# Performance work log

Hardware: AMD Instinct MI355X
Metric: run time of the kernel (lower is better)

The kernel has to match this reference:

```python
import jax, jax.numpy as jnp
import numpy as np
import math

NUM_HEADS = 8
Q_STRIDE = 2
KV_STRIDE = 2
POS_MAG = 1.0
WAVE_LEN = 1000.0


def _pos_embedding(h, w, h_kv, w_kv, feat_dim):
    # sinusoidal embedding of coordinate differences (in input-resolution units)
    h_idxs = jnp.arange(h, dtype=jnp.float32) * Q_STRIDE
    w_idxs = jnp.arange(w, dtype=jnp.float32) * Q_STRIDE
    h_kv_idxs = jnp.arange(h_kv, dtype=jnp.float32) * KV_STRIDE
    w_kv_idxs = jnp.arange(w_kv, dtype=jnp.float32) * KV_STRIDE
    h_diff = (h_idxs[:, None] - h_kv_idxs[None, :]) * POS_MAG  # [h, h_kv]
    w_diff = (w_idxs[:, None] - w_kv_idxs[None, :]) * POS_MAG  # [w, w_kv]
    feat_range = jnp.arange(feat_dim // 4, dtype=jnp.float32)
    dim_mat = WAVE_LEN ** (4.0 / feat_dim * feat_range)       # [feat_dim/4]
    ang_x = w_diff[:, :, None] / dim_mat                       # [w, w_kv, feat_dim/4]
    ang_y = h_diff[:, :, None] / dim_mat                       # [h, h_kv, feat_dim/4]
    emb_x = jnp.concatenate([jnp.sin(ang_x), jnp.cos(ang_x)], axis=2)  # [w, w_kv, feat_dim/2]
    emb_y = jnp.concatenate([jnp.sin(ang_y), jnp.cos(ang_y)], axis=2)  # [h, h_kv, feat_dim/2]
    return emb_x, emb_y


def setup_inputs() -> dict:
    key = jax.random.key(0)
    ks = jax.random.split(key, 10)
    n, C, H, W = 2, 256, 96, 96
    s = 0.05
    return {
        "x": jax.random.normal(ks[0], (n, C, H, W), jnp.float32),
        "Wq": jax.random.normal(ks[1], (C, C), jnp.float32) * s,
        "Wk": jax.random.normal(ks[2], (C, C), jnp.float32) * s,
        "Wv": jax.random.normal(ks[3], (C, C), jnp.float32) * s,
        "Wx": jax.random.normal(ks[4], (C, C // 2), jnp.float32) * s,
        "Wy": jax.random.normal(ks[5], (C, C // 2), jnp.float32) * s,
        "appr_bias": jax.random.normal(ks[6], (C,), jnp.float32) * s,
        "Wp": jax.random.normal(ks[7], (C, C), jnp.float32) * s,
        "bp": jax.random.normal(ks[8], (C,), jnp.float32) * s,
        "gamma": jax.random.normal(ks[9], (1,), jnp.float32),
    }


def reference(x, Wq, Wk, Wv, Wx, Wy, appr_bias, Wp, bp, gamma):
    n, C, H, W = x.shape
    g = NUM_HEADS
    d = C // g  # qk_embed_dim == v_dim
    # AvgPool2d(kernel_size=1, stride=s) == strided subsampling
    x_q = x[:, :, ::Q_STRIDE, ::Q_STRIDE]
    x_kv = x[:, :, ::KV_STRIDE, ::KV_STRIDE]
    h, w = x_q.shape[2], x_q.shape[3]
    h_kv, w_kv = x_kv.shape[2], x_kv.shape[3]

    # 1x1 convs (no bias) == channel matmuls
    q = jnp.einsum('oc,nchw->nohw', Wq, x_q)   # [n, C, h, w]
    k = jnp.einsum('oc,nchw->nohw', Wk, x_kv)  # [n, C, h_kv, w_kv]
    v = jnp.einsum('oc,nchw->nohw', Wv, x_kv)  # [n, C, h_kv, w_kv]

    emb_x, emb_y = _pos_embedding(h, w, h_kv, w_kv, C)
    inv_sqrt2 = 1.0 / math.sqrt(2.0)
    # Linear(feat_dim/2 -> C), split into heads, scale by 1/sqrt(2)
    pos_x = (jnp.einsum('wvf,of->wvo', emb_x, Wx).reshape(w, w_kv, g, d)
             .transpose(2, 0, 1, 3)) * inv_sqrt2  # [g, w, w_kv, d]
    pos_y = (jnp.einsum('huf,of->huo', emb_y, Wy).reshape(h, h_kv, g, d)
             .transpose(2, 0, 1, 3)) * inv_sqrt2  # [g, h, h_kv, d]

    qr = q.reshape(n, g, d, h, w).transpose(0, 1, 3, 4, 2)  # [n, g, h, w, d]
    kr = k.reshape(n, g, d, h_kv * w_kv)                     # [n, g, d, kv]

    # bias . key term, broadcast over query positions
    e_key = jnp.einsum('gd,ngdk->ngk', appr_bias.reshape(g, d), kr)
    e_key = e_key.reshape(n, g, 1, 1, h_kv, w_kv)
    # query . pos_x term (broadcast over h_kv), query . pos_y term (broadcast over w_kv)
    e_x = jnp.einsum('nghwd,gwvd->nghwv', qr, pos_x)[:, :, :, :, None, :]
    e_y = jnp.einsum('nghwd,ghud->nghwu', qr, pos_y)[:, :, :, :, :, None]

    energy = (e_key + e_x + e_y).reshape(n, g, h * w, h_kv * w_kv)
    attn = jax.nn.softmax(energy, axis=-1)  # [n, g, hw, kv]

    vr = v.reshape(n, g, d, h_kv * w_kv)  # [n, g, d, kv]
    out = jnp.einsum('ngqk,ngdk->ngdq', attn, vr).reshape(n, C, h, w)

    out = jnp.einsum('oc,nchw->nohw', Wp, out) + bp[None, :, None, None]
    out = jax.image.resize(out, (n, C, H, W), method='bilinear')
    return gamma * out + x
```

## Files before the change

### kernel.cpp

```cpp
#include <hip/hip_runtime.h>
#include <hip/hip_bf16.h>
#include <math.h>

#define NB 2
#define CC 256
#define NPOS 2304
#define NDELTA 95

typedef __attribute__((ext_vector_type(8))) short short8;
typedef __attribute__((ext_vector_type(4))) float floatx4;

__device__ inline unsigned short f2bf(float x) {
    unsigned int u = __float_as_uint(x);
    u = (u + 0x7FFFu + ((u >> 16) & 1u)) >> 16;
    return (unsigned short)u;
}
__device__ inline float bf2f(unsigned short h) {
    return __uint_as_float(((unsigned int)h) << 16);
}
__device__ inline unsigned int pk2(float a, float b) {
    return (unsigned int)f2bf(a) | ((unsigned int)f2bf(b) << 16);
}
__device__ inline unsigned int pkmul(unsigned int a, unsigned int b) {
    __hip_bfloat162 x = *(__hip_bfloat162*)&a;
    __hip_bfloat162 y = *(__hip_bfloat162*)&b;
    __hip_bfloat162 r = __hmul2(x, y);
    return *(unsigned int*)&r;
}

__global__ __launch_bounds__(256) void prep_extract_kernel(
    const float* __restrict__ Wx, const float* __restrict__ Wy,
    const float* __restrict__ Wk, const float* __restrict__ ab,
    const float* __restrict__ Wq, const float* __restrict__ Wv,
    const float* __restrict__ Wp, const float* __restrict__ x,
    unsigned short* __restrict__ posxb, unsigned short* __restrict__ posyb,
    unsigned short* __restrict__ Wb, unsigned short* __restrict__ Wpb,
    unsigned short* __restrict__ xs_t)
{
    __shared__ __align__(16) unsigned short Lt[64][264];
    int b = blockIdx.x;
    int t = threadIdx.x;
    if (b < NDELTA) {
        float* emb = (float*)&Lt[0][0];
        float delta = (float)(b - 47);
        if (t < 64) {
            float dim_inv = exp2f(-(float)t * 0.15571537944784511f);
            float ang = 2.0f * delta * dim_inv;
            emb[t]      = sinf(ang);
            emb[t + 64] = cosf(ang);
        }
        __syncthreads();
        float4 sx4 = {0.f,0.f,0.f,0.f}, sy4 = {0.f,0.f,0.f,0.f};
        const float4* wxr = (const float4*)(Wx + t * 128);
        const float4* wyr = (const float4*)(Wy + t * 128);
        const float4* e4  = (const float4*)emb;
        for (int f = 0; f < 32; ++f) {
            float4 e = e4[f], a = wxr[f], bb = wyr[f];
            sx4.x += e.x * a.x;  sx4.y += e.y * a.y;
            sx4.z += e.z * a.z;  sx4.w += e.w * a.w;
            sy4.x += e.x * bb.x; sy4.y += e.y * bb.y;
            sy4.z += e.z * bb.z; sy4.w += e.w * bb.w;
        }
        float sx = (sx4.x + sx4.y) + (sx4.z + sx4.w);
        float sy = (sy4.x + sy4.y) + (sy4.z + sy4.w);
        const float inv_sqrt2 = 0.70710678118654752440f;
        int g = t >> 5, d = t & 31;
        posxb[((size_t)g * 96 + b) * 32 + d] = f2bf(sx * inv_sqrt2);
        posyb[((size_t)g * 96 + b) * 32 + d] = f2bf(sy * inv_sqrt2);
    } else if (b == NDELTA) {
        int g = t >> 5, d = t & 31;
        posxb[((size_t)g * 96 + 95) * 32 + d] = 0;
        posyb[((size_t)g * 96 + 95) * 32 + d] = 0;
    } else if (b < 96 + 640) {
        int o = b - 96;
        float v = 0.f;
        if (o < 256)      v = Wq[o * 256 + t];
        else if (o < 512) v = Wv[(o - 256) * 256 + t];
        else if (o < 520) {
            int g = o - 512;
            float s = 0.f;
            for (int d = 0; d < 32; ++d)
                s += ab[g * 32 + d] * Wk[(g * 32 + d) * 256 + t];
            v = s;
        }
        Wb[(size_t)o * 256 + t] = f2bf(v);
    } else if (b < 992) {
        int o = b - 736;
        Wpb[(size_t)o * 256 + t] = f2bf(Wp[o * 256 + t]);
    } else {
        int blk = b - 992;
        int pt = blk % 36;
        int n = blk / 36;
        int p0 = pt * 64;
        int cw = t >> 4;
        int pl = t & 15;

        for (int cc = 0; cc < 16; ++cc) {
            int c = cc * 16 + cw;
            const float* src = x + ((size_t)(n * 256 + c)) * (96 * 96);
            #pragma unroll
            for (int k = 0; k < 4; ++k) {
                int p = p0 + pl + k * 16;
                int i = p / 48, j = p - i * 48;
                Lt[pl + k * 16][c] = f2bf(src[(2 * i) * 96 + 2 * j]);
            }
        }
        __syncthreads();
        #pragma unroll
        for (int it = 0; it < 8; ++it) {
            int s = t + it * 256;
            int p = s >> 5, c8 = s & 31;
            uint4 v = *(const uint4*)&Lt[p][c8 * 8];
            *(uint4*)(xs_t + ((size_t)(n * NPOS + p0 + p)) * 256 + c8 * 8) = v;
        }
    }
}

__global__ __launch_bounds__(256, 2) void qkvh_kernel(
    const unsigned short* __restrict__ xs_t, const unsigned short* __restrict__ Wb,
    unsigned short* __restrict__ qbuf, uint4* __restrict__ vhat)
{
    __shared__ __align__(16) unsigned short Vt[4][33][72];
    int mT = blockIdx.x;
    int nT = blockIdx.y;
    int t = threadIdx.x;
    int wm = t >> 6, L = t & 63, l16 = L & 15, oct = L >> 4;
    int colBase = nT * 64;
    int n = colBase / NPOS;
    int p0 = colBase - n * NPOS;
    int o_w = mT * 128 + wm * 32;
    bool isV = (mT >= 2);
    int gv = (mT & 1) * 4 + wm;

    const unsigned short* A0 = Wb + (size_t)(o_w + l16) * 256 + oct * 8;
    const unsigned short* A1 = A0 + 16 * 256;
    const unsigned short* AE = Wb + (size_t)(512 + gv) * 256 + oct * 8;
    const unsigned short* B0 = xs_t + ((size_t)(n * NPOS + p0 + l16)) * 256 + oct * 8;

    floatx4 acc[2][4] = {};
    floatx4 accE[4] = {};
    #pragma unroll
    for (int kc = 0; kc < 8; ++kc) {
        int k0 = kc * 32;
        short8 a0 = *(const short8*)(A0 + k0);
        short8 a1 = *(const short8*)(A1 + k0);
        short8 b0 = *(const short8*)(B0 + k0);
        short8 b1 = *(const short8*)(B0 + 16 * 256 + k0);
        short8 b2 = *(const short8*)(B0 + 32 * 256 + k0);
        short8 b3 = *(const short8*)(B0 + 48 * 256 + k0);
        acc[0][0] = __builtin_amdgcn_mfma_f32_16x16x32_bf16(a0, b0, acc[0][0], 0, 0, 0);
        acc[0][1] = __builtin_amdgcn_mfma_f32_16x16x32_bf16(a0, b1, acc[0][1], 0, 0, 0);
        acc[0][2] = __builtin_amdgcn_mfma_f32_16x16x32_bf16(a0, b2, acc[0][2], 0, 0, 0);
        acc[0][3] = __builtin_amdgcn_mfma_f32_16x16x32_bf16(a0, b3, acc[0][3], 0, 0, 0);
        acc[1][0] = __builtin_amdgcn_mfma_f32_16x16x32_bf16(a1, b0, acc[1][0], 0, 0, 0);
        acc[1][1] = __builtin_amdgcn_mfma_f32_16x16x32_bf16(a1, b1, acc[1][1], 0, 0, 0);
        acc[1][2] = __builtin_amdgcn_mfma_f32_16x16x32_bf16(a1, b2, acc[1][2], 0, 0, 0);
        acc[1][3] = __builtin_amdgcn_mfma_f32_16x16x32_bf16(a1, b3, acc[1][3], 0, 0, 0);
        if (isV) {
            short8 ae = *(const short8*)(AE + k0);
            accE[0] = __builtin_amdgcn_mfma_f32_16x16x32_bf16(ae, b0, accE[0], 0, 0, 0);
            accE[1] = __builtin_amdgcn_mfma_f32_16x16x32_bf16(ae, b1, accE[1], 0, 0, 0);
            accE[2] = __builtin_amdgcn_mfma_f32_16x16x32_bf16(ae, b2, accE[2], 0, 0, 0);
            accE[3] = __builtin_amdgcn_mfma_f32_16x16x32_bf16(ae, b3, accE[3], 0, 0, 0);
        }
    }

    if (!isV) {
        #pragma unroll
        for (int af = 0; af < 2; ++af) {
            int ob = o_w + af * 16 + oct * 4;
            int gq = ob >> 5, d0 = ob & 31;
            #pragma unroll
            for (int f = 0; f < 4; ++f) {
                int p = p0 + f * 16 + l16;
                uint2 w;
                w.x = pk2(acc[af][f][0], acc[af][f][1]);
                w.y = pk2(acc[af][f][2], acc[af][f][3]);
                *(uint2*)&qbuf[((size_t)(n * 8 + gq) * NPOS + p) * 32 + d0] = w;
            }
        }
    } else {
        #pragma unroll
        for (int f = 0; f < 4; ++f) {
            float e = __expf(accE[f][0]);
            #pragma unroll
            for (int af = 0; af < 2; ++af)
                #pragma unroll
                for (int r = 0; r < 4; ++r)
                    Vt[wm][af * 16 + oct * 4 + r][f * 16 + l16] =
                        f2bf(acc[af][f][r] * e);
            if (oct == 0)
                Vt[wm][32][f * 16 + l16] = f2bf(e);
        }
        __syncthreads();

        int i = L >> 3, j = L & 7;
        int K = p0 + 8 * i;
        int tile = K / 96;
        int rem = K - tile * 96;
        int cc = rem >> 5;
        int lhi = (rem & 31) >> 3;
        uint4* vout = vhat + ((size_t)(n * 8 + gv) * 24 + tile) * 576;
        #pragma unroll
        for (int mm = 0; mm < 4; ++mm) {
            int d = j + 8 * mm;
            int nn = d >> 4;
            int Ls = lhi * 16 + (d & 15);
            uint4 w = *(const uint4*)&Vt[wm][d][8 * i];
            vout[(cc * 3 + nn) * 64 + Ls] = w;
        }
        {
            uint4 wa = (j == 0) ? *(const uint4*)&Vt[wm][32][8 * i]
                                : make_uint4(0u, 0u, 0u, 0u);
            vout[(cc * 3 + 2) * 64 + lhi * 16 + j] = wa;
            vout[(cc * 3 + 2) * 64 + lhi * 16 + j + 8] = make_uint4(0u, 0u, 0u, 0u);
        }
    }
}

#define DO_TILE(BB, TT) do {                                                   \
    int u0_ = (TT) * 2;                                                        \
    unsigned int y0_ = Ys[qp * 50 + u0_];     y0_ |= y0_ << 16;                \
    unsigned int y1_ = Ys[qp * 50 + u0_ + 1]; y1_ |= y1_ << 16;                \
    unsigned int Yc0_ = y0_, Yc1_ = (o < 2) ? y0_ : y1_, Yc2_ = y1_;           \
    union { unsigned int u[4]; short8 s; } av_;                                \
    av_.u[0] = pkmul(Xp[0], Yc0_); av_.u[1] = pkmul(Xp[1], Yc0_);              \
    av_.u[2] = pkmul(Xp[2], Yc0_); av_.u[3] = pkmul(Xp[3], Yc0_);              \
    acc0 = __builtin_amdgcn_mfma_f32_16x16x32_bf16(av_.s, *(const short8*)&BB[0], acc0, 0, 0, 0); \
    acc1 = __builtin_amdgcn_mfma_f32_16x16x32_bf16(av_.s, *(const short8*)&BB[1], acc1, 0, 0, 0); \
    acc2 = __builtin_amdgcn_mfma_f32_16x16x32_bf16(av_.s, *(const short8*)&BB[2], acc2, 0, 0, 0); \
    av_.u[0] = pkmul(Xp[4], Yc1_); av_.u[1] = pkmul(Xp[5], Yc1_);              \
    av_.u[2] = pkmul(Xp[6], Yc1_); av_.u[3] = pkmul(Xp[7], Yc1_);              \
    acc0 = __builtin_amdgcn_mfma_f32_16x16x32_bf16(av_.s, *(const short8*)&BB[3], acc0, 0, 0, 0); \
    acc1 = __builtin_amdgcn_mfma_f32_16x16x32_bf16(av_.s, *(const short8*)&BB[4], acc1, 0, 0, 0); \
    acc2 = __builtin_amdgcn_mfma_f32_16x16x32_bf16(av_.s, *(const short8*)&BB[5], acc2, 0, 0, 0); \
    av_.u[0] = pkmul(Xp[8], Yc2_); av_.u[1] = pkmul(Xp[9], Yc2_);              \
    av_.u[2] = pkmul(Xp[10], Yc2_); av_.u[3] = pkmul(Xp[11], Yc2_);            \
    acc0 = __builtin_amdgcn_mfma_f32_16x16x32_bf16(av_.s, *(const short8*)&BB[6], acc0, 0, 0, 0); \
    acc1 = __builtin_amdgcn_mfma_f32_16x16x32_bf16(av_.s, *(const short8*)&BB[7], acc1, 0, 0, 0); \
    acc2 = __builtin_amdgcn_mfma_f32_16x16x32_bf16(av_.s, *(const short8*)&BB[8], acc2, 0, 0, 0); \
} while (0)

__global__ __launch_bounds__(256, 3) void attn_kernel(
    const unsigned short* __restrict__ qbuf, const unsigned short* __restrict__ posxb,
    const unsigned short* __restrict__ posyb, const uint4* __restrict__ vhat,
    unsigned short* __restrict__ oattn_t)
{
    __shared__ unsigned short Xs[64 * 50];
    __shared__ unsigned short Ys[64 * 50];
    __shared__ float linv_s[64];

    int blk = blockIdx.x;
    int qt = blk % 36;
    int ng = blk / 36;
    int nb = ng >> 3, g = ng & 7;
    int qbase = qt * 64;
    int t = threadIdx.x;
    int m = t >> 6, L = t & 63;
    int l16 = L & 15, oct = L >> 4;

    {
        int qtile0 = qbase + m * 16;
        int hq = qtile0 / 48;
        int wq0 = qtile0 - hq * 48;
        short8 aq = *(const short8*)(qbuf +
            ((size_t)ng * NPOS + qtile0 + l16) * 32 + oct * 8);
        const unsigned short* pxg = posxb + (size_t)g * 96 * 32;
        const unsigned short* pyg = posyb + (size_t)g * 96 * 32;
        floatx4 zero = {0.f, 0.f, 0.f, 0.f};
        #pragma unroll
        for (int j = 0; j < 6; ++j) {
            int dl = j * 16 + l16;
            short8 bx = *(const short8*)(pxg + (size_t)dl * 32 + oct * 8);
            short8 by = *(const short8*)(pyg + (size_t)dl * 32 + oct * 8);
            floatx4 tx = __builtin_amdgcn_mfma_f32_16x16x32_bf16(aq, bx, zero, 0, 0, 0);
            floatx4 ty = __builtin_amdgcn_mfma_f32_16x16x32_bf16(aq, by, zero, 0, 0, 0);
            int u = hq + 47 - dl;
            bool uok = (u >= 0) && (u < 48);
            #pragma unroll
            for (int r = 0; r < 4; ++r) {
                int ql = oct * 4 + r;
                int v = wq0 + ql + 47 - dl;
                if (v >= 0 && v < 48)
                    Xs[(m * 16 + ql) * 50 + v] = f2bf(__expf(tx[r]));
                if (uok)
                    Ys[(m * 16 + ql) * 50 + u] = f2bf(__expf(ty[r]));
            }
        }
    }
    __syncthreads();

    int qp = m * 16 + l16;
    int o = oct;
    unsigned int Xp[12];
    #pragma unroll
    for (int c = 0; c < 3; ++c)
        #pragma unroll
        for (int jj = 0; jj < 4; ++jj) {
            int k = c * 32 + o * 8 + jj * 2;
            int v0 = (k < 48) ? k : k - 48;
            Xp[c * 4 + jj] = *(const unsigned int*)&Xs[qp * 50 + v0];
        }

    floatx4 acc0 = {0.f, 0.f, 0.f, 0.f};
    floatx4 acc1 = {0.f, 0.f, 0.f, 0.f};
    floatx4 acc2 = {0.f, 0.f, 0.f, 0.f};

    const uint4* vb = vhat + (size_t)ng * 24 * 576 + L;
    uint4 Abuf[9], Bbuf[9];
    #pragma unroll
    for (int gg = 0; gg < 9; ++gg) Abuf[gg] = vb[gg * 64];

    for (int tile = 0; tile < 24; tile += 2) {
        const uint4* sB = vb + (tile + 1) * 576;
        #pragma unroll
        for (int gg = 0; gg < 9; ++gg) Bbuf[gg] = sB[gg * 64];
        DO_TILE(Abuf, tile);
        if (tile + 2 < 24) {
            const uint4* sA = vb + (tile + 2) * 576;
            #pragma unroll
            for (int gg = 0; gg < 9; ++gg) Abuf[gg] = sA[gg * 64];
        }
        DO_TILE(Bbuf, tile + 1);
    }

    if ((L & 15) == 0) {
        int qc = m * 16 + (L >> 4) * 4;
        #pragma unroll
        for (int r = 0; r < 4; ++r)
            linv_s[qc + r] = 1.0f / acc2[r];
    }
    __syncthreads();
    {
        int qc = m * 16 + (L >> 4) * 4;
        int d0 = L & 15;
        #pragma unroll
        for (int r = 0; r < 4; ++r) {
            float lir = linv_s[qc + r];
            size_t row = ((size_t)nb * NPOS + qbase + qc + r) * 256;
            oattn_t[row + g * 32 + d0]      = f2bf(acc0[r] * lir);
            oattn_t[row + g * 32 + 16 + d0] = f2bf(acc1[r] * lir);
        }
    }
}

__global__ __launch_bounds__(256, 2) void proj_kernel(
    const unsigned short* __restrict__ oattn_t, const unsigned short* __restrict__ Wpb,
    const float* __restrict__ bpv, unsigned short* __restrict__ projb)
{
    int mT = blockIdx.x;
    int nT = blockIdx.y;
    int t = threadIdx.x;
    int wm = t >> 6, L = t & 63, l16 = L & 15, oct = L >> 4;
    int colBase = nT * 64;
    int n = colBase / NPOS;
    int p0 = colBase - n * NPOS;
    int o_w = mT * 128 + wm * 32;

    const unsigned short* A0 = Wpb + (size_t)(o_w + l16) * 256 + oct * 8;
    const unsigned short* A1 = A0 + 16 * 256;
    const unsigned short* B0 = oattn_t + ((size_t)(n * NPOS + p0 + l16)) * 256 + oct * 8;

    floatx4 acc[2][4] = {};
    #pragma unroll
    for (int kc = 0; kc < 8; ++kc) {
        int k0 = kc * 32;
        short8 a0 = *(const short8*)(A0 + k0);
        short8 a1 = *(const short8*)(A1 + k0);
        short8 b0 = *(const short8*)(B0 + k0);
        short8 b1 = *(const short8*)(B0 + 16 * 256 + k0);
        short8 b2 = *(const short8*)(B0 + 32 * 256 + k0);
        short8 b3 = *(const short8*)(B0 + 48 * 256 + k0);
        acc[0][0] = __builtin_amdgcn_mfma_f32_16x16x32_bf16(a0, b0, acc[0][0], 0, 0, 0);
        acc[0][1] = __builtin_amdgcn_mfma_f32_16x16x32_bf16(a0, b1, acc[0][1], 0, 0, 0);
        acc[0][2] = __builtin_amdgcn_mfma_f32_16x16x32_bf16(a0, b2, acc[0][2], 0, 0, 0);
        acc[0][3] = __builtin_amdgcn_mfma_f32_16x16x32_bf16(a0, b3, acc[0][3], 0, 0, 0);
        acc[1][0] = __builtin_amdgcn_mfma_f32_16x16x32_bf16(a1, b0, acc[1][0], 0, 0, 0);
        acc[1][1] = __builtin_amdgcn_mfma_f32_16x16x32_bf16(a1, b1, acc[1][1], 0, 0, 0);
        acc[1][2] = __builtin_amdgcn_mfma_f32_16x16x32_bf16(a1, b2, acc[1][2], 0, 0, 0);
        acc[1][3] = __builtin_amdgcn_mfma_f32_16x16x32_bf16(a1, b3, acc[1][3], 0, 0, 0);
    }

    #pragma unroll
    for (int af = 0; af < 2; ++af) {
        #pragma unroll
        for (int f = 0; f < 4; ++f) {
            int p = p0 + f * 16 + l16;
            #pragma unroll
            for (int r = 0; r < 4; ++r) {
                int o = o_w + af * 16 + oct * 4 + r;
                projb[((size_t)(n * 256 + o)) * NPOS + p] = f2bf(acc[af][f][r] + bpv[o]);
            }
        }
    }
}

__global__ __launch_bounds__(256) void resize_kernel(
    const unsigned short* __restrict__ projb, const float* __restrict__ x,
    const float* __restrict__ gamma, float* __restrict__ out)
{
    int idx4 = blockIdx.x * 256 + threadIdx.x;
    int J0 = (idx4 % 24) * 4;
    int tmp = idx4 / 24;
    int I = tmp % 96;
    int nc = tmp / 96;

    int jr = I >> 1;
    int r0, r1; float w0, w1;
    if ((I & 1) == 0) { r0 = (jr > 0) ? jr - 1 : 0; r1 = jr; w0 = 0.25f; w1 = 0.75f; }
    else              { r0 = jr; r1 = (jr < 47) ? jr + 1 : 47; w0 = 0.75f; w1 = 0.25f; }

    int jcb = J0 >> 1;
    int cm1 = (jcb > 0) ? jcb - 1 : 0;
    int c2  = jcb + 2;

    const unsigned short* P = projb + (size_t)nc * NPOS;
    const unsigned short* Pr0 = P + r0 * 48;
    const unsigned short* Pr1 = P + r1 * 48;
    float a0 = bf2f(Pr0[cm1]),   a1 = bf2f(Pr0[jcb]);
    float a2 = bf2f(Pr0[jcb+1]), a3 = bf2f(Pr0[c2]);
    float b0 = bf2f(Pr1[cm1]),   b1 = bf2f(Pr1[jcb]);
    float b2 = bf2f(Pr1[jcb+1]), b3 = bf2f(Pr1[c2]);

    float hA[4], hB[4];
    hA[0] = 0.25f * a0 + 0.75f * a1;  hB[0] = 0.25f * b0 + 0.75f * b1;
    hA[1] = 0.75f * a1 + 0.25f * a2;  hB[1] = 0.75f * b1 + 0.25f * b2;
    hA[2] = 0.25f * a1 + 0.75f * a2;  hB[2] = 0.25f * b1 + 0.75f * b2;
    hA[3] = 0.75f * a2 + 0.25f * a3;  hB[3] = 0.75f * b2 + 0.25f * b3;

    size_t base = ((size_t)nc * 96 + I) * 96 + J0;
    float4 xv = *(const float4*)(x + base);
    float gm = gamma[0];
    float4 ov;
    ov.x = gm * (w0 * hA[0] + w1 * hB[0]) + xv.x;
    ov.y = gm * (w0 * hA[1] + w1 * hB[1]) + xv.y;
    ov.z = gm * (w0 * hA[2] + w1 * hB[2]) + xv.z;
    ov.w = gm * (w0 * hA[3] + w1 * hB[3]) + xv.w;
    *(float4*)(out + base) = ov;
}

extern "C" void kernel_launch(void* const* d_in, const int* in_sizes, int n_in,
                              void* d_out, int out_size, void* d_ws, size_t ws_size,
                              hipStream_t stream)
{
    const float* x     = (const float*)d_in[0];
    const float* Wq    = (const float*)d_in[1];
    const float* Wk    = (const float*)d_in[2];
    const float* Wv    = (const float*)d_in[3];
    const float* Wx    = (const float*)d_in[4];
    const float* Wy    = (const float*)d_in[5];
    const float* ab    = (const float*)d_in[6];
    const float* Wp    = (const float*)d_in[7];
    const float* bp    = (const float*)d_in[8];
    const float* gamma = (const float*)d_in[9];
    float* out = (float*)d_out;

    unsigned short* posxb = (unsigned short*)d_ws;
    unsigned short* posyb  = posxb + 8 * 96 * 32;
    unsigned short* Wb     = posyb + 8 * 96 * 32;
    unsigned short* Wpb    = Wb + (size_t)640 * 256;
    unsigned short* xs_t   = Wpb + (size_t)256 * 256;
    unsigned short* qbuf   = xs_t + (size_t)2 * NPOS * 256;
    unsigned short* oattn_t= qbuf + (size_t)2 * NPOS * 256;
    unsigned short* projb  = oattn_t + (size_t)2 * NPOS * 256;
    float* unused_vbuf = (float*)(projb + (size_t)2 * NPOS * 256);
    float* unused_ek   = unused_vbuf + (size_t)2 * 256 * NPOS;
    uint4* vhat  = (uint4*)(unused_ek + 16 * NPOS);

    hipLaunchKernelGGL(prep_extract_kernel, dim3(1064), dim3(256), 0, stream,
                       Wx, Wy, Wk, ab, Wq, Wv, Wp, x, posxb, posyb, Wb, Wpb, xs_t);
    hipLaunchKernelGGL(qkvh_kernel, dim3(4, 72), dim3(256), 0, stream,
                       xs_t, Wb, qbuf, vhat);
    hipLaunchKernelGGL(attn_kernel, dim3(576), dim3(256), 0, stream,
                       qbuf, posxb, posyb, vhat, oattn_t);
    hipLaunchKernelGGL(proj_kernel, dim3(2, 72), dim3(256), 0, stream,
                       oattn_t, Wpb, bp, projb);
    hipLaunchKernelGGL(resize_kernel, dim3((2 * 256 * 96 * 96) / (256 * 4)), dim3(256), 0, stream,
                       projb, x, gamma, out);
}
```

Baseline: 148.2 us.

## Fuse input extraction and weight conversion into QKV projection kernel

Merges the prep/extract kernel and the QKV projection kernel into a single front kernel. Each QKV block now subsamples x straight into LDS and converts the fp32 Wq/Wv rows to bf16 in registers, so the xs_t and Wb round trips through global memory and one launch go away. The cost is that the x subsampling gather is repeated four times (once per mT tile), and the bias-key weight reduction is recomputed in every V block. The positional embedding and Wp conversion tasks now share the grid with the projection blocks.

```diff
diff --git a/kernel.cpp b/kernel.cpp
--- a/kernel.cpp
+++ b/kernel.cpp
@@ -27,194 +27,190 @@
     __hip_bfloat162 r = __hmul2(x, y);
     return *(unsigned int*)&r;
 }
-
-__global__ __launch_bounds__(256) void prep_extract_kernel(
-    const float* __restrict__ Wx, const float* __restrict__ Wy,
-    const float* __restrict__ Wk, const float* __restrict__ ab,
-    const float* __restrict__ Wq, const float* __restrict__ Wv,
-    const float* __restrict__ Wp, const float* __restrict__ x,
+__device__ inline short8 ldA_f32(const float* __restrict__ p) {
+    float4 f0 = *(const float4*)p;
+    float4 f1 = *(const float4*)(p + 4);
+    union { unsigned int u[4]; short8 s; } r;
+    r.u[0] = pk2(f0.x, f0.y);
+    r.u[1] = pk2(f0.z, f0.w);
+    r.u[2] = pk2(f1.x, f1.y);
+    r.u[3] = pk2(f1.z, f1.w);
+    return r.s;
+}
+
+__global__ __launch_bounds__(256, 2) void front_kernel(
+    const float* __restrict__ x,  const float* __restrict__ Wq,
+    const float* __restrict__ Wv, const float* __restrict__ Wk,
+    const float* __restrict__ ab, const float* __restrict__ Wx,
+    const float* __restrict__ Wy, const float* __restrict__ Wp,
     unsigned short* __restrict__ posxb, unsigned short* __restrict__ posyb,
-    unsigned short* __restrict__ Wb, unsigned short* __restrict__ Wpb,
-    unsigned short* __restrict__ xs_t)
+    unsigned short* __restrict__ Wpb,
+    unsigned short* __restrict__ qbuf, uint4* __restrict__ vhat)
 {
-    __shared__ __align__(16) unsigned short Lt[64][264];
+    __shared__ __align__(16) unsigned char LDSraw[64 * 264 * 2];
+    __shared__ __align__(16) unsigned short We[4][256];
     int b = blockIdx.x;
     int t = threadIdx.x;
-    if (b < NDELTA) {
-        float* emb = (float*)&Lt[0][0];
-        float delta = (float)(b - 47);
-        if (t < 64) {
-            float dim_inv = exp2f(-(float)t * 0.15571537944784511f);
-            float ang = 2.0f * delta * dim_inv;
-            emb[t]      = sinf(ang);
-            emb[t + 64] = cosf(ang);
+
+    if (b < 288) {
+        unsigned short (*Lt)[264] = (unsigned short (*)[264])LDSraw;
+        int mT = b & 3;
+        int nT = b >> 2;
+        int wm = t >> 6, L = t & 63, l16 = L & 15, oct = L >> 4;
+        int colBase = nT * 64;
+        int n = colBase / NPOS;
+        int p0 = colBase - n * NPOS;
+        int o_w = mT * 128 + wm * 32;
+        bool isV = (mT >= 2);
+        int gv = (mT & 1) * 4 + wm;
+
+        {
+            int cw = t >> 4;
+            int pl = t & 15;
+            for (int cc = 0; cc < 16; ++cc) {
+                int c = cc * 16 + cw;
+                const float* src = x + ((size_t)(n * 256 + c)) * (96 * 96);
+                #pragma unroll
+                for (int k = 0; k < 4; ++k) {
+                    int p = p0 + pl + k * 16;
+                    int i = p / 48, j = p - i * 48;
+                    Lt[pl + k * 16][c] = f2bf(src[(2 * i) * 96 + 2 * j]);
+                }
+            }
+            if (isV) {
+                #pragma unroll
+                for (int ci = 0; ci < 4; ++ci) {
+                    int c = L + ci * 64;
+                    float s = 0.f;
+                    for (int d = 0; d < 32; ++d)
+                        s += ab[gv * 32 + d] * Wk[(gv * 32 + d) * 256 + c];
+                    We[wm][c] = f2bf(s);
+                }
+            }
         }
         __syncthreads();
-        float4 sx4 = {0.f,0.f,0.f,0.f}, sy4 = {0.f,0.f,0.f,0.f};
-        const float4* wxr = (const float4*)(Wx + t * 128);
-        const float4* wyr = (const float4*)(Wy + t * 128);
-        const float4* e4  = (const float4*)emb;
-        for (int f = 0; f < 32; ++f) {
-            float4 e = e4[f], a = wxr[f], bb = wyr[f];
-            sx4.x += e.x * a.x;  sx4.y += e.y * a.y;
-            sx4.z += e.z * a.z;  sx4.w += e.w * a.w;
-            sy4.x += e.x * bb.x; sy4.y += e.y * bb.y;
-            sy4.z += e.z * bb.z; sy4.w += e.w * bb.w;
-        }
-        float sx = (sx4.x + sx4.y) + (sx4.z + sx4.w);
-        float sy = (sy4.x + sy4.y) + (sy4.z + sy4.w);
-        const float inv_sqrt2 = 0.70710678118654752440f;
-        int g = t >> 5, d = t & 31;
-        posxb[((size_t)g * 96 + b) * 32 + d] = f2bf(sx * inv_sqrt2);
-        posyb[((size_t)g * 96 + b) * 32 + d] = f2bf(sy * inv_sqrt2);
-    } else if (b == NDELTA) {
-        int g = t >> 5, d = t & 31;
-        posxb[((size_t)g * 96 + 95) * 32 + d] = 0;
-        posyb[((size_t)g * 96 + 95) * 32 + d] = 0;
-    } else if (b < 96 + 640) {
-        int o = b - 96;
-        float v = 0.f;
-        if (o < 256)      v = Wq[o * 256 + t];
-        else if (o < 512) v = Wv[(o - 256) * 256 + t];
-        else if (o < 520) {
-            int g = o - 512;
-            float s = 0.f;
-            for (int d = 0; d < 32; ++d)
-                s += ab[g * 32 + d] * Wk[(g * 32 + d) * 256 + t];
-            v = s;
-        }
-        Wb[(size_t)o * 256 + t] = f2bf(v);
-    } else if (b < 992) {
-        int o = b - 736;
+
+        const float* Arow = isV ? (Wv + (size_t)(o_w - 256 + l16) * 256)
+                                : (Wq + (size_t)(o_w + l16) * 256);
+        floatx4 acc[2][4] = {};
+        floatx4 accE[4] = {};
+        #pragma unroll
+        for (int kc = 0; kc < 8; ++kc) {
+            int k0 = kc * 32;
+            int col = oct * 8 + k0;
+            short8 a0 = ldA_f32(Arow + col);
+            short8 a1 = ldA_f32(Arow + 16 * 256 + col);
+            short8 b0 = *(const short8*)&Lt[l16][col];
+            short8 b1 = *(const short8*)&Lt[l16 + 16][col];
+            short8 b2 = *(const short8*)&Lt[l16 + 32][col];
+            short8 b3 = *(const short8*)&Lt[l16 + 48][col];
+            acc[0][0] = __builtin_amdgcn_mfma_f32_16x16x32_bf16(a0, b0, acc[0][0], 0, 0, 0);
+            acc[0][1] = __builtin_amdgcn_mfma_f32_16x16x32_bf16(a0, b1, acc[0][1], 0, 0, 0);
+            acc[0][2] = __builtin_amdgcn_mfma_f32_16x16x32_bf16(a0, b2, acc[0][2], 0, 0, 0);
+            acc[0][3] = __builtin_amdgcn_mfma_f32_16x16x32_bf16(a0, b3, acc[0][3], 0, 0, 0);
+            acc[1][0] = __builtin_amdgcn_mfma_f32_16x16x32_bf16(a1, b0, acc[1][0], 0, 0, 0);
+            acc[1][1] = __builtin_amdgcn_mfma_f32_16x16x32_bf16(a1, b1, acc[1][1], 0, 0, 0);
+            acc[1][2] = __builtin_amdgcn_mfma_f32_16x16x32_bf16(a1, b2, acc[1][2], 0, 0, 0);
+            acc[1][3] = __builtin_amdgcn_mfma_f32_16x16x32_bf16(a1, b3, acc[1][3], 0, 0, 0);
+            if (isV) {
+                short8 ae = *(const short8*)&We[wm][col];
+                accE[0] = __builtin_amdgcn_mfma_f32_16x16x32_bf16(ae, b0, accE[0], 0, 0, 0);
+                accE[1] = __builtin_amdgcn_mfma_f32_16x16x32_bf16(ae, b1, accE[1], 0, 0, 0);
+                accE[2] = __builtin_amdgcn_mfma_f32_16x16x32_bf16(ae, b2, accE[2], 0, 0, 0);
+                accE[3] = __builtin_amdgcn_mfma_f32_16x16x32_bf16(ae, b3, accE[3], 0, 0, 0);
+            }
+        }
+
+        if (!isV) {
+            #pragma unroll
+            for (int af = 0; af < 2; ++af) {
+                int ob = o_w + af * 16 + oct * 4;
+                int gq = ob >> 5, d0 = ob & 31;
+                #pragma unroll
+                for (int f = 0; f < 4; ++f) {
+                    int p = p0 + f * 16 + l16;
+                    uint2 w;
+                    w.x = pk2(acc[af][f][0], acc[af][f][1]);
+                    w.y = pk2(acc[af][f][2], acc[af][f][3]);
+                    *(uint2*)&qbuf[((size_t)(n * 8 + gq) * NPOS + p) * 32 + d0] = w;
+                }
+            }
+        } else {
+            __syncthreads();
+            unsigned short (*Vt)[33][72] = (unsigned short (*)[33][72])LDSraw;
+            #pragma unroll
+            for (int f = 0; f < 4; ++f) {
+                float e = __expf(accE[f][0]);
+                #pragma unroll
+                for (int af = 0; af < 2; ++af)
+                    #pragma unroll
+                    for (int r = 0; r < 4; ++r)
+                        Vt[wm][af * 16 + oct * 4 + r][f * 16 + l16] =
+                            f2bf(acc[af][f][r] * e);
+                if (oct == 0)
+                    Vt[wm][32][f * 16 + l16] = f2bf(e);
+            }
+            __syncthreads();
+
+            int i = L >> 3, j = L & 7;
+            int K = p0 + 8 * i;
+            int tile = K / 96;
+            int rem = K - tile * 96;
+            int cc = rem >> 5;
+            int lhi = (rem & 31) >> 3;
+            uint4* vout = vhat + ((size_t)(n * 8 + gv) * 24 + tile) * 576;
+            #pragma unroll
+            for (int mm = 0; mm < 4; ++mm) {
+                int d = j + 8 * mm;
+                int nn = d >> 4;
+                int Ls = lhi * 16 + (d & 15);
+                uint4 w = *(const uint4*)&Vt[wm][d][8 * i];
+                vout[(cc * 3 + nn) * 64 + Ls] = w;
+            }
+            {
+                uint4 wa = (j == 0) ? *(const uint4*)&Vt[wm][32][8 * i]
+                                    : make_uint4(0u, 0u, 0u, 0u);
+                vout[(cc * 3 + 2) * 64 + lhi * 16 + j] = wa;
+                vout[(cc * 3 + 2) * 64 + lhi * 16 + j + 8] = make_uint4(0u, 0u, 0u, 0u);
+            }
+        }
+    } else if (b < 384) {
+        int task = b - 288;
+        if (task < NDELTA) {
+            float* emb = (float*)LDSraw;
+            float delta = (float)(task - 47);
+            if (t < 64) {
+                float dim_inv = exp2f(-(float)t * 0.15571537944784511f);
+                float ang = 2.0f * delta * dim_inv;
+                emb[t]      = sinf(ang);
+                emb[t + 64] = cosf(ang);
+            }
+            __syncthreads();
+            float4 sx4 = {0.f,0.f,0.f,0.f}, sy4 = {0.f,0.f,0.f,0.f};
+            const float4* wxr = (const float4*)(Wx + t * 128);
+            const float4* wyr = (const float4*)(Wy + t * 128);
+            const float4* e4  = (const float4*)emb;
+            for (int f = 0; f < 32; ++f) {
+                float4 e = e4[f], a = wxr[f], bb = wyr[f];
+                sx4.x += e.x * a.x;  sx4.y += e.y * a.y;
+                sx4.z += e.z * a.z;  sx4.w += e.w * a.w;
+                sy4.x += e.x * bb.x; sy4.y += e.y * bb.y;
+                sy4.z += e.z * bb.z; sy4.w += e.w * bb.w;
+            }
+            float sx = (sx4.x + sx4.y) + (sx4.z + sx4.w);
+            float sy = (sy4.x + sy4.y) + (sy4.z + sy4.w);
+            const float inv_sqrt2 = 0.70710678118654752440f;
+            int g = t >> 5, d = t & 31;
+            posxb[((size_t)g * 96 + task) * 32 + d] = f2bf(sx * inv_sqrt2);
+            posyb[((size_t)g * 96 + task) * 32 + d] = f2bf(sy * inv_sqrt2);
+        } else {
+            int g = t >> 5, d = t & 31;
+            posxb[((size_t)g * 96 + 95) * 32 + d] = 0;
+            posyb[((size_t)g * 96 + 95) * 32 + d] = 0;
+        }
+    } else {
+        int o = b - 384;
         Wpb[(size_t)o * 256 + t] = f2bf(Wp[o * 256 + t]);
-    } else {
-        int blk = b - 992;
-        int pt = blk % 36;
-        int n = blk / 36;
-        int p0 = pt * 64;
-        int cw = t >> 4;
-        int pl = t & 15;
-
-        for (int cc = 0; cc < 16; ++cc) {
-            int c = cc * 16 + cw;
-            const float* src = x + ((size_t)(n * 256 + c)) * (96 * 96);
-            #pragma unroll
-            for (int k = 0; k < 4; ++k) {
-                int p = p0 + pl + k * 16;
-                int i = p / 48, j = p - i * 48;
-                Lt[pl + k * 16][c] = f2bf(src[(2 * i) * 96 + 2 * j]);
-            }
-        }
-        __syncthreads();
-        #pragma unroll
-        for (int it = 0; it < 8; ++it) {
-            int s = t + it * 256;
-            int p = s >> 5, c8 = s & 31;
-            uint4 v = *(const uint4*)&Lt[p][c8 * 8];
-            *(uint4*)(xs_t + ((size_t)(n * NPOS + p0 + p)) * 256 + c8 * 8) = v;
-        }
-    }
-}
-
-__global__ __launch_bounds__(256, 2) void qkvh_kernel(
-    const unsigned short* __restrict__ xs_t, const unsigned short* __restrict__ Wb,
-    unsigned short* __restrict__ qbuf, uint4* __restrict__ vhat)
-{
-    __shared__ __align__(16) unsigned short Vt[4][33][72];
-    int mT = blockIdx.x;
-    int nT = blockIdx.y;
-    int t = threadIdx.x;
-    int wm = t >> 6, L = t & 63, l16 = L & 15, oct = L >> 4;
-    int colBase = nT * 64;
-    int n = colBase / NPOS;
-    int p0 = colBase - n * NPOS;
-    int o_w = mT * 128 + wm * 32;
-    bool isV = (mT >= 2);
-    int gv = (mT & 1) * 4 + wm;
-
-    const unsigned short* A0 = Wb + (size_t)(o_w + l16) * 256 + oct * 8;
-    const unsigned short* A1 = A0 + 16 * 256;
-    const unsigned short* AE = Wb + (size_t)(512 + gv) * 256 + oct * 8;
-    const unsigned short* B0 = xs_t + ((size_t)(n * NPOS + p0 + l16)) * 256 + oct * 8;
-
-    floatx4 acc[2][4] = {};
-    floatx4 accE[4] = {};
-    #pragma unroll
-    for (int kc = 0; kc < 8; ++kc) {
-        int k0 = kc * 32;
-        short8 a0 = *(const short8*)(A0 + k0);
-        short8 a1 = *(const short8*)(A1 + k0);
-        short8 b0 = *(const short8*)(B0 + k0);
-        short8 b1 = *(const short8*)(B0 + 16 * 256 + k0);
-        short8 b2 = *(const short8*)(B0 + 32 * 256 + k0);
-        short8 b3 = *(const short8*)(B0 + 48 * 256 + k0);
-        acc[0][0] = __builtin_amdgcn_mfma_f32_16x16x32_bf16(a0, b0, acc[0][0], 0, 0, 0);
-        acc[0][1] = __builtin_amdgcn_mfma_f32_16x16x32_bf16(a0, b1, acc[0][1], 0, 0, 0);
-        acc[0][2] = __builtin_amdgcn_mfma_f32_16x16x32_bf16(a0, b2, acc[0][2], 0, 0, 0);
-        acc[0][3] = __builtin_amdgcn_mfma_f32_16x16x32_bf16(a0, b3, acc[0][3], 0, 0, 0);
-        acc[1][0] = __builtin_amdgcn_mfma_f32_16x16x32_bf16(a1, b0, acc[1][0], 0, 0, 0);
-        acc[1][1] = __builtin_amdgcn_mfma_f32_16x16x32_bf16(a1, b1, acc[1][1], 0, 0, 0);
-        acc[1][2] = __builtin_amdgcn_mfma_f32_16x16x32_bf16(a1, b2, acc[1][2], 0, 0, 0);
-        acc[1][3] = __builtin_amdgcn_mfma_f32_16x16x32_bf16(a1, b3, acc[1][3], 0, 0, 0);
-        if (isV) {
-            short8 ae = *(const short8*)(AE + k0);
-            accE[0] = __builtin_amdgcn_mfma_f32_16x16x32_bf16(ae, b0, accE[0], 0, 0, 0);
-            accE[1] = __builtin_amdgcn_mfma_f32_16x16x32_bf16(ae, b1, accE[1], 0, 0, 0);
-            accE[2] = __builtin_amdgcn_mfma_f32_16x16x32_bf16(ae, b2, accE[2], 0, 0, 0);
-            accE[3] = __builtin_amdgcn_mfma_f32_16x16x32_bf16(ae, b3, accE[3], 0, 0, 0);
-        }
-    }
-
-    if (!isV) {
-        #pragma unroll
-        for (int af = 0; af < 2; ++af) {
-            int ob = o_w + af * 16 + oct * 4;
-            int gq = ob >> 5, d0 = ob & 31;
-            #pragma unroll
-            for (int f = 0; f < 4; ++f) {
-                int p = p0 + f * 16 + l16;
-                uint2 w;
-                w.x = pk2(acc[af][f][0], acc[af][f][1]);
-                w.y = pk2(acc[af][f][2], acc[af][f][3]);
-                *(uint2*)&qbuf[((size_t)(n * 8 + gq) * NPOS + p) * 32 + d0] = w;
-            }
-        }
-    } else {
-        #pragma unroll
-        for (int f = 0; f < 4; ++f) {
-            float e = __expf(accE[f][0]);
-            #pragma unroll
-            for (int af = 0; af < 2; ++af)
-                #pragma unroll
-                for (int r = 0; r < 4; ++r)
-                    Vt[wm][af * 16 + oct * 4 + r][f * 16 + l16] =
-                        f2bf(acc[af][f][r] * e);
-            if (oct == 0)
-                Vt[wm][32][f * 16 + l16] = f2bf(e);
-        }
-        __syncthreads();
-
-        int i = L >> 3, j = L & 7;
-        int K = p0 + 8 * i;
-        int tile = K / 96;
-        int rem = K - tile * 96;
-        int cc = rem >> 5;
-        int lhi = (rem & 31) >> 3;
-        uint4* vout = vhat + ((size_t)(n * 8 + gv) * 24 + tile) * 576;
-        #pragma unroll
-        for (int mm = 0; mm < 4; ++mm) {
-            int d = j + 8 * mm;
-            int nn = d >> 4;
-            int Ls = lhi * 16 + (d & 15);
-            uint4 w = *(const uint4*)&Vt[wm][d][8 * i];
-            vout[(cc * 3 + nn) * 64 + Ls] = w;
-        }
-        {
-            uint4 wa = (j == 0) ? *(const uint4*)&Vt[wm][32][8 * i]
-                                : make_uint4(0u, 0u, 0u, 0u);
-            vout[(cc * 3 + 2) * 64 + lhi * 16 + j] = wa;
-            vout[(cc * 3 + 2) * 64 + lhi * 16 + j + 8] = make_uint4(0u, 0u, 0u, 0u);
-        }
     }
 }
 
@@ -457,20 +453,15 @@
 
     unsigned short* posxb = (unsigned short*)d_ws;
     unsigned short* posyb  = posxb + 8 * 96 * 32;
-    unsigned short* Wb     = posyb + 8 * 96 * 32;
-    unsigned short* Wpb    = Wb + (size_t)640 * 256;
-    unsigned short* xs_t   = Wpb + (size_t)256 * 256;
-    unsigned short* qbuf   = xs_t + (size_t)2 * NPOS * 256;
+    unsigned short* Wpb    = posyb + 8 * 96 * 32;
+    unsigned short* qbuf   = Wpb + (size_t)256 * 256;
     unsigned short* oattn_t= qbuf + (size_t)2 * NPOS * 256;
     unsigned short* projb  = oattn_t + (size_t)2 * NPOS * 256;
-    float* unused_vbuf = (float*)(projb + (size_t)2 * NPOS * 256);
-    float* unused_ek   = unused_vbuf + (size_t)2 * 256 * NPOS;
-    uint4* vhat  = (uint4*)(unused_ek + 16 * NPOS);
-
-    hipLaunchKernelGGL(prep_extract_kernel, dim3(1064), dim3(256), 0, stream,
-                       Wx, Wy, Wk, ab, Wq, Wv, Wp, x, posxb, posyb, Wb, Wpb, xs_t);
-    hipLaunchKernelGGL(qkvh_kernel, dim3(4, 72), dim3(256), 0, stream,
-                       xs_t, Wb, qbuf, vhat);
+    uint4* vhat  = (uint4*)(projb + (size_t)2 * NPOS * 256);
+
+    hipLaunchKernelGGL(front_kernel, dim3(640), dim3(256), 0, stream,
+                       x, Wq, Wv, Wk, ab, Wx, Wy, Wp,
+                       posxb, posyb, Wpb, qbuf, vhat);
     hipLaunchKernelGGL(attn_kernel, dim3(576), dim3(256), 0, stream,
                        qbuf, posxb, posyb, vhat, oattn_t);
     hipLaunchKernelGGL(proj_kernel, dim3(2, 72), dim3(256), 0, stream,
```

Measured after the change: 143.8 us. -3.0%, faster.
